# Optimization experiments

Hardware: AMD Instinct MI355X
Metric: run time of the kernel (lower is better)

## Reference

```python
import jax, jax.numpy as jnp
import numpy as np

INPUT_SIZE = 512
HIDDEN = 1024
N_QP = 64
M_QP = 128
QP_ITER = 50
MIN_EIG = 0.01
N_P = N_QP * (N_QP + 1) // 2              # 2080
N_H = M_QP * N_QP                          # 8192
N_OUT = N_P + N_QP + N_H + M_QP            # 10464
BATCH = 1024


def setup_inputs() -> dict:
    key = jax.random.key(0)
    ks = jax.random.split(key, 4)
    s = lambda fan_in: np.float32(1.0 / np.sqrt(fan_in))
    return {
        "x": jax.random.normal(ks[0], (BATCH, INPUT_SIZE), jnp.float32),
        "W1": jax.random.normal(ks[1], (INPUT_SIZE, HIDDEN), jnp.float32) * s(INPUT_SIZE),
        "b1": jnp.zeros((HIDDEN,), jnp.float32),
        "W2": jax.random.normal(ks[2], (HIDDEN, HIDDEN), jnp.float32) * s(HIDDEN),
        "b2": jnp.zeros((HIDDEN,), jnp.float32),
        "W3": jax.random.normal(ks[3], (HIDDEN, N_OUT), jnp.float32) * s(HIDDEN),
        "b3": jnp.zeros((N_OUT,), jnp.float32),
    }


def _make_psd(p):
    # p: (bs, n(n+1)/2) packed row-major lower triangle of Cholesky factor L.
    # Diagonal entries (index i(i+1)/2 - 1) -> sqrt(min_eig) + softplus, so P = L L' is PSD.
    bs = p.shape[0]
    i = jnp.arange(1, N_QP + 1)
    diag_idx = i * (i + 1) // 2 - 1
    p = p.at[:, diag_idx].set(np.float32(np.sqrt(MIN_EIG)) + jax.nn.softplus(p[:, diag_idx]))
    r, c = jnp.tril_indices(N_QP)
    L = jnp.zeros((bs, N_QP, N_QP), p.dtype).at[:, r, c].set(p)
    return jnp.einsum('bik,bjk->bij', L, L)


def _forward(x, W1, b1, W2, b2, W3, b3):
    # MLP generating QP parameters (P, q, H, b)
    h = jax.nn.relu(x @ W1 + b1)
    h = jax.nn.relu(h @ W2 + b2)
    out = h @ W3 + b3                               # (bs, N_OUT)
    P_params = out[:, :N_P]
    q = out[:, N_P:N_P + N_QP]                      # (bs, n)
    H = out[:, N_P + N_QP:N_P + N_QP + N_H].reshape(-1, M_QP, N_QP)  # (bs, m, n)
    b = out[:, N_P + N_QP + N_H:]                   # (bs, m)
    P = _make_psd(P_params)                         # (bs, n, n)

    # Step sizes: tau = sigma = 0.9 / ||H||_2, spectral norm via 10 fixed power iterations
    v = jnp.ones((x.shape[0], N_QP), x.dtype) / np.float32(np.sqrt(N_QP))
    for _ in range(10):
        w = jnp.einsum('bmn,bm->bn', H, jnp.einsum('bmn,bn->bm', H, v))
        v = w / (jnp.linalg.norm(w, axis=1, keepdims=True) + 1e-12)
    sn = jnp.linalg.norm(jnp.einsum('bmn,bn->bm', H, v), axis=1) + 1e-6
    tau = (0.9 / sn)[:, None]                       # (bs, 1) primal step
    sig = tau                                       # dual step

    # Precompute (I + tau P)^{-1} once; fixed across PDHG iterations
    eye = jnp.eye(N_QP, dtype=x.dtype)
    Minv = jnp.linalg.inv(eye[None] + tau[:, :, None] * P)

    x0 = jnp.zeros((x.shape[0], N_QP), x.dtype)
    lam0 = jnp.zeros((x.shape[0], M_QP), x.dtype)

    def step(carry, _):
        xp, xbar, lam = carry
        lam = jax.nn.relu(lam - sig * (jnp.einsum('bmn,bn->bm', H, xbar) + b))
        xn = jnp.einsum('bnk,bk->bn', Minv, xp + tau * (jnp.einsum('bmn,bm->bn', H, lam) - q))
        return (xn, 2.0 * xn - xp, lam), None

    (xs, _, _), _ = jax.lax.scan(step, (x0, x0, lam0), None, length=QP_ITER)
    return xs  # (bs, n_qp): last primal iterate, matching solver(...)[1][:, -1, :]


def reference(x, W1, b1, W2, b2, W3, b3):
    return _forward(x, W1, b1, W2, b2, W3, b3)
```

## Files before the change

### kernel.cpp

```cpp
#include <hip/hip_runtime.h>
#include <cstdint>

typedef unsigned short u16;
typedef __attribute__((ext_vector_type(8))) short short8;
typedef __attribute__((ext_vector_type(4))) float floatx4;
typedef __attribute__((ext_vector_type(4))) float f4;

#define NQP   64
#define MQP   128
#define NP    2080
#define NHH   8192
#define NOUT  10464
#define NOUTP 10496

__device__ __forceinline__ float b2f(u16 u) {
  union { unsigned int i; float f; } v; v.i = ((unsigned int)u) << 16; return v.f;
}
__device__ __forceinline__ u16 f2b(float f) {
  union { float f; unsigned int i; } v; v.f = f;
  unsigned int r = v.i + 0x7fffu + ((v.i >> 16) & 1u);
  return (u16)(r >> 16);
}

__global__ __launch_bounds__(256) void detect_dtype(const u16* __restrict__ w,
                                                    int* __restrict__ flag) {
  __shared__ int cnt;
  if (threadIdx.x == 0) cnt = 0;
  __syncthreads();
  int c = 0;
  for (int i = threadIdx.x; i < 16384; i += 256) {
    const int e = (w[i] >> 7) & 0xFF;
    if (e >= 130 || e <= 90) ++c;
  }
  atomicAdd(&cnt, c);
  __syncthreads();
  if (threadIdx.x == 0) flag[0] = (cnt > 3000) ? 1 : 0;
}

__device__ __forceinline__ u16 load_elem_bf16(const void* p, size_t idx, int isf32) {
  return isf32 ? f2b(((const float*)p)[idx]) : ((const u16*)p)[idx];
}

__global__ __launch_bounds__(256) void convert_bf16(const void* __restrict__ in,
                                                    u16* __restrict__ out, int n,
                                                    const int* __restrict__ flag) {
  const int isf = flag[0];
  for (int i = blockIdx.x * 256 + threadIdx.x; i < n; i += gridDim.x * 256)
    out[i] = load_elem_bf16(in, i, isf);
}

__global__ __launch_bounds__(256) void conv_biases(const void* __restrict__ b1,
                                                   const void* __restrict__ b2,
                                                   const void* __restrict__ b3,
                                                   float* __restrict__ bf1,
                                                   float* __restrict__ bf2,
                                                   float* __restrict__ bf3,
                                                   const int* __restrict__ flag) {
  const int isf = flag[0];
  const int i = blockIdx.x * 256 + threadIdx.x;
  if (i < 1024) {
    bf1[i] = isf ? ((const float*)b1)[i] : b2f(((const u16*)b1)[i]);
  } else if (i < 2048) {
    const int j = i - 1024;
    bf2[j] = isf ? ((const float*)b2)[j] : b2f(((const u16*)b2)[j]);
  } else if (i < 2048 + NOUT) {
    const int j = i - 2048;
    bf3[j] = isf ? ((const float*)b3)[j] : b2f(((const u16*)b3)[j]);
  }
}

__global__ __launch_bounds__(256) void transpose_all(const void* __restrict__ W1,
                                                     const void* __restrict__ W2,
                                                     const void* __restrict__ W3,
                                                     u16* __restrict__ W1t,
                                                     u16* __restrict__ W2t,
                                                     u16* __restrict__ W3t,
                                                     const int* __restrict__ flag) {
  const int bx = blockIdx.x, by = blockIdx.y;
  const void* in; u16* out; int K, N, Npad, bxo;
  if (bx < 32)      { in = W1; out = W1t; K = 512;  N = 1024; Npad = 1024;  bxo = 0;
                      if (by >= 16) return; }
  else if (bx < 64) { in = W2; out = W2t; K = 1024; N = 1024; Npad = 1024;  bxo = 32; }
  else              { in = W3; out = W3t; K = 1024; N = NOUT; Npad = NOUTP; bxo = 64; }
  __shared__ u16 tile[32][33];
  const int isf = flag[0];
  const int n0 = (bx - bxo) * 32, k0 = by * 32;
  const int tx = threadIdx.x & 31, ty = threadIdx.x >> 5;
// ... 100 lines not shown
__global__ __launch_bounds__(256) void gemm_bt64(const u16* __restrict__ Ahi, const u16* __restrict__ Alo,
                                                 const u16* __restrict__ Bt,  const float* __restrict__ bias,
                                                 u16* __restrict__ Chi, u16* __restrict__ Clo,
                                                 int N, int K) {
  __shared__ __align__(16) u16 lA[64 * 32];
  __shared__ __align__(16) u16 lAlo[64 * 32];
  __shared__ __align__(16) u16 lB[64 * 32];
  const int tile_n = blockIdx.x * 64;
  const int tile_m = blockIdx.y * 64;
  const int lane = threadIdx.x & 63;
  const int wv   = threadIdx.x >> 6;
  const int wm = (wv & 1) * 32;
  const int wn = (wv >> 1) * 32;
  const int sr = lane >> 2;
  const int sk = (lane & 3) * 8;
  floatx4 acc[2][2] = {};

  for (int k0 = 0; k0 < K; k0 += 32) {
    {
      const int r = wv * 16 + sr;
      gload_lds16(Ahi + (size_t)(tile_m + r) * K + k0 + sk, lA + wv * 512);
      if (HAS_LO)
        gload_lds16(Alo + (size_t)(tile_m + r) * K + k0 + sk, lAlo + wv * 512);
      gload_lds16(Bt + (size_t)(tile_n + r) * K + k0 + sk, lB + wv * 512);
    }
    __syncthreads();
    const int ro = lane & 15;
    const int qo = (lane >> 4) * 8;
    short8 af[2], bfr[2], al[2];
#pragma unroll
    for (int i = 0; i < 2; ++i) af[i] = *(const short8*)(lA + (wm + i * 16 + ro) * 32 + qo);
#pragma unroll
    for (int j = 0; j < 2; ++j) bfr[j] = *(const short8*)(lB + (wn + j * 16 + ro) * 32 + qo);
    if (HAS_LO) {
#pragma unroll
      for (int i = 0; i < 2; ++i) al[i] = *(const short8*)(lAlo + (wm + i * 16 + ro) * 32 + qo);
    }
#pragma unroll
    for (int i = 0; i < 2; ++i)
#pragma unroll
      for (int j = 0; j < 2; ++j) {
        acc[i][j] = __builtin_amdgcn_mfma_f32_16x16x32_bf16(af[i], bfr[j], acc[i][j], 0, 0, 0);
        if (HAS_LO)
          acc[i][j] = __builtin_amdgcn_mfma_f32_16x16x32_bf16(al[i], bfr[j], acc[i][j], 0, 0, 0);
      }
    __syncthreads();
  }

  const int colb = tile_n + wn + (lane & 15);
  const int rowb = tile_m + wm + (lane >> 4) * 4;
#pragma unroll
  for (int j = 0; j < 2; ++j) {
    const int col = colb + j * 16;
    const float bv = bias[col];
#pragma unroll
    for (int i = 0; i < 2; ++i) {
#pragma unroll
      for (int v = 0; v < 4; ++v) {
        const int row = rowb + i * 16 + v;
        float val = acc[i][j][v] + bv;
        val = fmaxf(val, 0.f);
        const u16 hi = f2b(val);
        Chi[(size_t)row * N + col] = hi;
        if (EPI == 0) {
          const float lo = val - b2f(hi);
          Clo[(size_t)row * N + col] = f2b(lo);
        }
      }
    }
  }
}

__device__ __forceinline__ f4 ld4s(const float* p) { return *(const f4*)p; }
__device__ __forceinline__ void st4s(float* p, f4 v) { *(f4*)p = v; }
__device__ __forceinline__ float dot4(f4 a, f4 b) {
  return fmaf(a.x, b.x, fmaf(a.y, b.y, fmaf(a.z, b.z, a.w * b.w)));
}
__device__ __forceinline__ f4 shx4(f4 v, int m) {
  f4 r;
  r.x = __shfl_xor(v.x, m, 64); r.y = __shfl_xor(v.y, m, 64);
  r.z = __shfl_xor(v.z, m, 64); r.w = __shfl_xor(v.w, m, 64);
  return r;
}
__device__ __forceinline__ int hQ(int m, int g) {
  return (m << 6) + (((g ^ (m & 15))) << 2);
}

__global__ __launch_bounds__(256, 4) void qp_solve(const float* __restrict__ outbuf,
                                                   void* __restrict__ xs,
                                                   const int* __restrict__ flag) {
  __shared__ __align__(16) float H_s[8192];
  __shared__ __align__(16) float lam_s[128];
  __shared__ __align__(16) float b_s[128];
  __shared__ __align__(16) float part_s[4][64];
  __shared__ __align__(16) float rhs_s[64];
  __shared__ __align__(16) float xb_s[64];
  __shared__ __align__(16) float xp_s[64];
  __shared__ __align__(16) float q_s[64];
  __shared__ __align__(16) float buf2[2][64];
  __shared__ float tau_sh;

  const int t = threadIdx.x;
  const int w = t >> 6, l = t & 63;
  const int am = 32 * w + (l >> 1), as = l & 1;
  const int bg = l & 15, bc = l >> 4;
  const int ci = 16 * w + (l >> 2), cc = l & 3;
  const int isf = flag[0];
  const float* ob = outbuf + (size_t)blockIdx.x * NOUT;

  float* Ld = H_s;
  float* ps = H_s + 4352;
  for (int e = t; e < 4352; e += 256) Ld[e] = 0.f;
  for (int e = t; e < NP; e += 256) ps[e] = ob[e];
  if (t < 64) q_s[t] = ob[NP + t];
  if (t >= 128 && t < 256) b_s[t - 128] = ob[NP + NQP + NHH + (t - 128)];
  __syncthreads();
  if (t < 64) {
    const int i = t + 1;
    const int d = i * (i + 1) / 2 - 1;
    const float xv = ps[d];
    ps[d] = 0.1f + (fmaxf(xv, 0.f) + log1pf(expf(-fabsf(xv))));
  }
  __syncthreads();
  for (int e = t; e < NP; e += 256) {
    int i = (int)((sqrtf(8.f * (float)e + 1.f) - 1.f) * 0.5f);
    while ((i + 1) * (i + 2) / 2 <= e) ++i;
    while (i * (i + 1) / 2 > e) --i;
    const int j = e - i * (i + 1) / 2;
    Ld[i * 68 + j] = ps[e];
  }
  __syncthreads();

  float M[16];
#pragma unroll
  for (int jj = 0; jj < 16; ++jj) M[jj] = 0.f;
#pragma unroll
  for (int h = 0; h < 2; ++h) {
    f4 Lr[8];
#pragma unroll
    for (int g = 0; g < 8; ++g) Lr[g] = ld4s(&Ld[ci * 68 + (h * 8 + g) * 4]);
#pragma unroll
    for (int jj = 0; jj < 16; ++jj) {
      const int j = 16 * cc + jj;
      float s = 0.f;
#pragma unroll
      for (int g = 0; g < 8; ++g) s += dot4(Lr[g], ld4s(&Ld[j * 68 + (h * 8 + g) * 4]));
      M[jj] += s;
    }
  }
  __syncthreads();

  for (int e = t; e < NHH; e += 256) {
    const int m = e >> 6, n = e & 63;
    H_s[hQ(m, n >> 2) + (n & 3)] = ob[NP + NQP + e];
  }
  if (t < 64) xb_s[t] = 0.125f;
  __syncthreads();

  for (int pi = 0; pi < 10; ++pi) {
    {
      float s = 0.f;
#pragma unroll
      for (int k = 0; k < 8; ++k) {
        const int g = 8 * as + k;
        s += dot4(ld4s(&H_s[hQ(am, g)]), ld4s(&xb_s[4 * g]));
      }
      s += __shfl_xor(s, 1, 64);
      if (as == 0) lam_s[am] = s;
    }
    __syncthreads();
    {
      f4 u = {0.f, 0.f, 0.f, 0.f};
#pragma unroll
      for (int k = 0; k < 8; ++k) {
        const int m = 32 * w + 8 * bc + k;
        u += ld4s(&H_s[hQ(m, bg)]) * lam_s[m];
      }
      u += shx4(u, 16); u += shx4(u, 32);
      if (l < 16) st4s(&part_s[w][4 * bg], u);
    }
    __syncthreads();
    if (t < 64) {
      const float u = part_s[0][t] + part_s[1][t] + part_s[2][t] + part_s[3][t];
      float ss = u * u;
#pragma unroll
      for (int o = 1; o <= 32; o <<= 1) ss += __shfl_xor(ss, o, 64);
      xb_s[t] = u / (sqrtf(ss) + 1e-12f);
    }
    __syncthreads();
  }
  {
    float s = 0.f;
#pragma unroll
    for (int k = 0; k < 8; ++k) {
      const int g = 8 * as + k;
      s += dot4(ld4s(&H_s[hQ(am, g)]), ld4s(&xb_s[4 * g]));
    }
    s += __shfl_xor(s, 1, 64);
    if (as == 0) lam_s[am] = s;
  }
  __syncthreads();
  if (t < 64) {
    const float a = lam_s[t], bb = lam_s[t + 64];
    float ss = a * a + bb * bb;
#pragma unroll
    for (int o = 1; o <= 32; o <<= 1) ss += __shfl_xor(ss, o, 64);
    if (t == 0) tau_sh = 0.9f / (sqrtf(ss) + 1e-6f);
  }
  __syncthreads();
  const float tau = tau_sh;

#pragma unroll
  for (int jj = 0; jj < 16; ++jj)
    M[jj] = tau * M[jj] + ((16 * cc + jj == ci) ? 1.0f : 0.0f);

  if (ci == 0) {
#pragma unroll
    for (int jj = 0; jj < 16; ++jj) buf2[0][16 * cc + jj] = M[jj];
  }
  __syncthreads();
#pragma unroll
  for (int k = 0; k < 64; ++k) {
    const int kb = k & 1;
    const int kc = k >> 4;
    const float d = 1.0f / buf2[kb][k];
    f4 rv[4];
#pragma unroll
    for (int u = 0; u < 4; ++u) rv[u] = ld4s(&buf2[kb][16 * cc + 4 * u]);
    const float f = __shfl(M[k & 15], (l & 60) | kc, 64);
    if (ci == k) {
#pragma unroll
      for (int jj = 0; jj < 16; ++jj) M[jj] = rv[jj >> 2][jj & 3] * d;
      if (cc == kc) M[k & 15] = d;
    } else {
#pragma unroll
      for (int jj = 0; jj < 16; ++jj)
        M[jj] = fmaf(-f, rv[jj >> 2][jj & 3] * d, M[jj]);
      if (cc == kc) M[k & 15] = -f * d;
    }
    if (k < 63 && ci == k + 1) {
#pragma unroll
      for (int jj = 0; jj < 16; ++jj) buf2[1 - kb][16 * cc + jj] = M[jj];
    }
    __syncthreads();
  }

  float c0;
  {
    float acc = 0.f;
#pragma unroll
    for (int u = 0; u < 4; ++u) {
      const f4 qv = ld4s(&q_s[16 * cc + 4 * u]);
      acc = fmaf(M[4 * u + 0], qv.x, acc);
      acc = fmaf(M[4 * u + 1], qv.y, acc);
      acc = fmaf(M[4 * u + 2], qv.z, acc);
      acc = fmaf(M[4 * u + 3], qv.w, acc);
    }
    acc += __shfl_xor(acc, 1, 64);
    acc += __shfl_xor(acc, 2, 64);
    c0 = tau * acc;
  }

  if (t < 64) { xb_s[t] = 0.f; xp_s[t] = 0.f; }
  float lam = 0.f, xpr = 0.f;
  const float br = b_s[am];
  __syncthreads();

  for (int it = 0; it < 50; ++it) {
    {
      float s = 0.f;
#pragma unroll
      for (int k = 0; k < 8; ++k) {
        const int g = 8 * as + k;
        s += dot4(ld4s(&H_s[hQ(am, g)]), ld4s(&xb_s[4 * g]));
      }
      s += __shfl_xor(s, 1, 64);
      lam = fmaxf(lam - tau * (s + br), 0.f);
      if (as == 0) lam_s[am] = lam;
    }
    __syncthreads();
    {
      f4 u = {0.f, 0.f, 0.f, 0.f};
#pragma unroll
      for (int k = 0; k < 8; ++k) {
        const int m = 32 * w + 8 * bc + k;
        u += ld4s(&H_s[hQ(m, bg)]) * lam_s[m];
      }
      u += shx4(u, 16); u += shx4(u, 32);
      if (l < 16) st4s(&part_s[w][4 * bg], u);
    }
    __syncthreads();
    if (t < 64) {
      const float uu = part_s[0][t] + part_s[1][t] + part_s[2][t] + part_s[3][t];
      rhs_s[t] = xp_s[t] + tau * uu;
    }
    __syncthreads();
    {
      float acc = 0.f;
#pragma unroll
      for (int u = 0; u < 4; ++u) {
        const f4 rv = ld4s(&rhs_s[16 * cc + 4 * u]);
        acc = fmaf(M[4 * u + 0], rv.x, acc);
        acc = fmaf(M[4 * u + 1], rv.y, acc);
        acc = fmaf(M[4 * u + 2], rv.z, acc);
        acc = fmaf(M[4 * u + 3], rv.w, acc);
      }
      acc += __shfl_xor(acc, 1, 64);
      acc += __shfl_xor(acc, 2, 64);
      if (cc == 0) {
        const float xn = acc - c0;
        xp_s[ci] = xn;
        xb_s[ci] = 2.f * xn - xpr;
        xpr = xn;
      }
    }
    __syncthreads();
  }

  if (cc == 0) {
    const size_t oi = (size_t)blockIdx.x * NQP + ci;
    if (isf) ((float*)xs)[oi] = xpr;
    else     ((u16*)xs)[oi]   = f2b(xpr);
  }
}

extern "C" void kernel_launch(void* const* d_in, const int* in_sizes, int n_in,
                              void* d_out, int out_size, void* d_ws, size_t ws_size,
                              hipStream_t stream) {
  const void* x  = d_in[0];
  const void* W1 = d_in[1];
  const void* b1 = d_in[2];
  const void* W2 = d_in[3];
  const void* b2 = d_in[4];
  const void* W3 = d_in[5];
  const void* b3 = d_in[6];

  char* ws = (char*)d_ws;
  size_t off = 0;
  auto take = [&](size_t bytes) -> char* {
    char* r = ws + off;
    off += (bytes + 255) & ~(size_t)255;
    return r;
  };
  int*   flag = (int*)take(256);
  float* bf1  = (float*)take(1024 * 4);
  float* bf2  = (float*)take(1024 * 4);
  float* bf3  = (float*)take((size_t)NOUT * 4);
  u16*   W3t  = (u16*)take((size_t)NOUTP * 1024 * 2);
  u16*   h2hi = (u16*)take(1024ull * 1024 * 2);
  char*  region = take(1024ull * NOUT * 4);
  float* outf = (float*)region;
  u16* xb   = (u16*)(region + 0);
  u16* W1t  = (u16*)(region + (1u << 20));
  u16* W2t  = (u16*)(region + (2u << 20));
  u16* h1hi = (u16*)(region + (4u << 20));
  u16* h1lo = (u16*)(region + (6u << 20));
  (void)ws_size; (void)in_sizes; (void)n_in; (void)out_size;

  detect_dtype<<<dim3(1), 256, 0, stream>>>((const u16*)W1, flag);

  convert_bf16<<<dim3(512), 256, 0, stream>>>(x, xb, 1024 * 512, flag);
  conv_biases<<<dim3(49), 256, 0, stream>>>(b1, b2, b3, bf1, bf2, bf3, flag);
  transpose_all<<<dim3(392, 32), 256, 0, stream>>>(W1, W2, W3, W1t, W2t, W3t, flag);

  gemm_bt64<0, false><<<dim3(16, 16), 256, 0, stream>>>(xb, nullptr, W1t, bf1,
                                                        h1hi, h1lo, 1024, 512);
  gemm_bt64<2, true><<<dim3(16, 16), 256, 0, stream>>>(h1hi, h1lo, W2t, bf2,
                                                       h2hi, nullptr, 1024, 1024);
  gemm_bt<1, false><<<dim3(NOUTP / 128, 8), 256, 0, stream>>>(h2hi, nullptr, W3t, bf3,
                                                              nullptr, nullptr, outf, 1024, NOUT, 1024);
  qp_solve<<<dim3(1024), 256, 0, stream>>>(outf, d_out, flag);
}
```

Measured before the change: 466.6 us.

## Store QP constraint matrix H in LDS as bf16 to double occupancy

The per-batch constraint matrix H is converted to bf16 and stored in shared memory with a new XOR swizzle. This halves its LDS footprint so launch bounds can be raised from 4 to 8 blocks per CU. The smaller scratch buffers (b_s, rhs_s) are removed by reusing lam_s and reading b straight from global memory. The cost is extra conversion work in the inner loops and reduced precision in H across the 50 PDHG iterations and the power iteration, which may drift from the fp32 reference.

```diff
diff --git a/kernel.cpp b/kernel.cpp
--- a/kernel.cpp
+++ b/kernel.cpp
@@ -3,6 +3,7 @@
 
 typedef unsigned short u16;
 typedef __attribute__((ext_vector_type(8))) short short8;
+typedef __attribute__((ext_vector_type(4))) short shortx4;
 typedef __attribute__((ext_vector_type(4))) float floatx4;
 typedef __attribute__((ext_vector_type(4))) float f4;
 
@@ -269,18 +270,24 @@
   r.z = __shfl_xor(v.z, m, 64); r.w = __shfl_xor(v.w, m, 64);
   return r;
 }
-__device__ __forceinline__ int hQ(int m, int g) {
-  return (m << 6) + (((g ^ (m & 15))) << 2);
-}
-
-__global__ __launch_bounds__(256, 4) void qp_solve(const float* __restrict__ outbuf,
+__device__ __forceinline__ float dot8h(short8 h, f4 a, f4 b) {
+  float s = b2f((u16)h[0]) * a.x;
+  s = fmaf(b2f((u16)h[1]), a.y, s);
+  s = fmaf(b2f((u16)h[2]), a.z, s);
+  s = fmaf(b2f((u16)h[3]), a.w, s);
+  s = fmaf(b2f((u16)h[4]), b.x, s);
+  s = fmaf(b2f((u16)h[5]), b.y, s);
+  s = fmaf(b2f((u16)h[6]), b.z, s);
+  s = fmaf(b2f((u16)h[7]), b.w, s);
+  return s;
+}
+
+__global__ __launch_bounds__(256, 8) void qp_solve(const float* __restrict__ outbuf,
                                                    void* __restrict__ xs,
                                                    const int* __restrict__ flag) {
-  __shared__ __align__(16) float H_s[8192];
+  __shared__ __align__(16) float Hreg[4352];
   __shared__ __align__(16) float lam_s[128];
-  __shared__ __align__(16) float b_s[128];
   __shared__ __align__(16) float part_s[4][64];
-  __shared__ __align__(16) float rhs_s[64];
   __shared__ __align__(16) float xb_s[64];
   __shared__ __align__(16) float xp_s[64];
   __shared__ __align__(16) float q_s[64];
@@ -294,27 +301,23 @@
   const int ci = 16 * w + (l >> 2), cc = l & 3;
   const int isf = flag[0];
   const float* ob = outbuf + (size_t)blockIdx.x * NOUT;
-
-  float* Ld = H_s;
-  float* ps = H_s + 4352;
+  u16* Hb = (u16*)Hreg;
+
+  float* Ld = Hreg;
   for (int e = t; e < 4352; e += 256) Ld[e] = 0.f;
-  for (int e = t; e < NP; e += 256) ps[e] = ob[e];
   if (t < 64) q_s[t] = ob[NP + t];
-  if (t >= 128 && t < 256) b_s[t - 128] = ob[NP + NQP + NHH + (t - 128)];
-  __syncthreads();
-  if (t < 64) {
-    const int i = t + 1;
-    const int d = i * (i + 1) / 2 - 1;
-    const float xv = ps[d];
-    ps[d] = 0.1f + (fmaxf(xv, 0.f) + log1pf(expf(-fabsf(xv))));
-  }
   __syncthreads();
   for (int e = t; e < NP; e += 256) {
     int i = (int)((sqrtf(8.f * (float)e + 1.f) - 1.f) * 0.5f);
     while ((i + 1) * (i + 2) / 2 <= e) ++i;
     while (i * (i + 1) / 2 > e) --i;
     const int j = e - i * (i + 1) / 2;
-    Ld[i * 68 + j] = ps[e];
+    Ld[i * 68 + j] = ob[e];
+  }
+  __syncthreads();
+  if (t < 64) {
+    const float xv = Ld[t * 68 + t];
+    Ld[t * 68 + t] = 0.1f + (fmaxf(xv, 0.f) + log1pf(expf(-fabsf(xv))));
   }
   __syncthreads();
 
@@ -337,20 +340,28 @@
   }
   __syncthreads();
 
-  for (int e = t; e < NHH; e += 256) {
-    const int m = e >> 6, n = e & 63;
-    H_s[hQ(m, n >> 2) + (n & 3)] = ob[NP + NQP + e];
+  for (int e = t; e < 4096; e += 256) {
+    const int m = e >> 5;
+    const int n = (e & 31) * 2;
+    const float f0 = ob[NP + NQP + m * 64 + n];
+    const float f1 = ob[NP + NQP + m * 64 + n + 1];
+    const int pc = (n >> 3) ^ (m & 7);
+    const int idx = (m << 6) + (pc << 3) + (n & 7);
+    *(unsigned int*)(Hb + idx) = (unsigned int)f2b(f0) | ((unsigned int)f2b(f1) << 16);
   }
   if (t < 64) xb_s[t] = 0.125f;
   __syncthreads();
+
+  const int am64 = am << 6, ax7 = am & 7;
 
   for (int pi = 0; pi < 10; ++pi) {
     {
       float s = 0.f;
 #pragma unroll
-      for (int k = 0; k < 8; ++k) {
-        const int g = 8 * as + k;
-        s += dot4(ld4s(&H_s[hQ(am, g)]), ld4s(&xb_s[4 * g]));
+      for (int c4 = 0; c4 < 4; ++c4) {
+        const int c = 4 * as + c4;
+        const short8 hv = *(const short8*)(Hb + am64 + ((c ^ ax7) << 3));
+        s += dot8h(hv, ld4s(&xb_s[8 * c]), ld4s(&xb_s[8 * c + 4]));
       }
       s += __shfl_xor(s, 1, 64);
       if (as == 0) lam_s[am] = s;
@@ -361,7 +372,12 @@
 #pragma unroll
       for (int k = 0; k < 8; ++k) {
         const int m = 32 * w + 8 * bc + k;
-        u += ld4s(&H_s[hQ(m, bg)]) * lam_s[m];
+        const shortx4 hv = *(const shortx4*)(Hb + (m << 6) + (((bg >> 1) ^ k) << 3) + ((bg & 1) << 2));
+        const float lm = lam_s[m];
+        u.x = fmaf(b2f((u16)hv.x), lm, u.x);
+        u.y = fmaf(b2f((u16)hv.y), lm, u.y);
+        u.z = fmaf(b2f((u16)hv.z), lm, u.z);
+        u.w = fmaf(b2f((u16)hv.w), lm, u.w);
       }
       u += shx4(u, 16); u += shx4(u, 32);
       if (l < 16) st4s(&part_s[w][4 * bg], u);
@@ -379,9 +395,10 @@
   {
     float s = 0.f;
 #pragma unroll
-    for (int k = 0; k < 8; ++k) {
-      const int g = 8 * as + k;
-      s += dot4(ld4s(&H_s[hQ(am, g)]), ld4s(&xb_s[4 * g]));
+    for (int c4 = 0; c4 < 4; ++c4) {
+      const int c = 4 * as + c4;
+      const short8 hv = *(const short8*)(Hb + am64 + ((c ^ ax7) << 3));
+      s += dot8h(hv, ld4s(&xb_s[8 * c]), ld4s(&xb_s[8 * c + 4]));
     }
     s += __shfl_xor(s, 1, 64);
     if (as == 0) lam_s[am] = s;
@@ -450,16 +467,17 @@
 
   if (t < 64) { xb_s[t] = 0.f; xp_s[t] = 0.f; }
   float lam = 0.f, xpr = 0.f;
-  const float br = b_s[am];
+  const float br = ob[NP + NQP + NHH + am];
   __syncthreads();
 
   for (int it = 0; it < 50; ++it) {
     {
       float s = 0.f;
 #pragma unroll
-      for (int k = 0; k < 8; ++k) {
-        const int g = 8 * as + k;
-        s += dot4(ld4s(&H_s[hQ(am, g)]), ld4s(&xb_s[4 * g]));
+      for (int c4 = 0; c4 < 4; ++c4) {
+        const int c = 4 * as + c4;
+        const short8 hv = *(const short8*)(Hb + am64 + ((c ^ ax7) << 3));
+        s += dot8h(hv, ld4s(&xb_s[8 * c]), ld4s(&xb_s[8 * c + 4]));
       }
       s += __shfl_xor(s, 1, 64);
       lam = fmaxf(lam - tau * (s + br), 0.f);
@@ -471,7 +489,12 @@
 #pragma unroll
       for (int k = 0; k < 8; ++k) {
         const int m = 32 * w + 8 * bc + k;
-        u += ld4s(&H_s[hQ(m, bg)]) * lam_s[m];
+        const shortx4 hv = *(const shortx4*)(Hb + (m << 6) + (((bg >> 1) ^ k) << 3) + ((bg & 1) << 2));
+        const float lm = lam_s[m];
+        u.x = fmaf(b2f((u16)hv.x), lm, u.x);
+        u.y = fmaf(b2f((u16)hv.y), lm, u.y);
+        u.z = fmaf(b2f((u16)hv.z), lm, u.z);
+        u.w = fmaf(b2f((u16)hv.w), lm, u.w);
       }
       u += shx4(u, 16); u += shx4(u, 32);
       if (l < 16) st4s(&part_s[w][4 * bg], u);
@@ -479,14 +502,14 @@
     __syncthreads();
     if (t < 64) {
       const float uu = part_s[0][t] + part_s[1][t] + part_s[2][t] + part_s[3][t];
-      rhs_s[t] = xp_s[t] + tau * uu;
+      lam_s[t] = xp_s[t] + tau * uu;
     }
     __syncthreads();
     {
       float acc = 0.f;
 #pragma unroll
       for (int u = 0; u < 4; ++u) {
-        const f4 rv = ld4s(&rhs_s[16 * cc + 4 * u]);
+        const f4 rv = ld4s(&lam_s[16 * cc + 4 * u]);
         acc = fmaf(M[4 * u + 0], rv.x, acc);
         acc = fmaf(M[4 * u + 1], rv.y, acc);
         acc = fmaf(M[4 * u + 2], rv.z, acc);
```

Result: slower. 582.3 us (+24.8%).

## Solve two QP problems per block to amortize barriers and raise ILP

Applied to the files above, without the earlier changes.

The QP solver kernel now processes two batch samples per 256-thread block, interleaving their matrix-vector products, Gauss-Jordan inversion and PDHG iterations. The goal is to halve the number of barrier-bound serial steps per sample and give each thread two independent dependency chains. In exchange, shared memory per block doubles to about 66KB and register pressure rises, which cuts occupancy (launch bounds drop to 2 blocks per SM). The grid also shrinks to 512 blocks, which can leave CUs underused.

```diff
diff --git a/kernel.cpp b/kernel.cpp
--- a/kernel.cpp
+++ b/kernel.cpp
@@ -273,19 +273,20 @@
   return (m << 6) + (((g ^ (m & 15))) << 2);
 }
 
-__global__ __launch_bounds__(256, 4) void qp_solve(const float* __restrict__ outbuf,
-                                                   void* __restrict__ xs,
-                                                   const int* __restrict__ flag) {
-  __shared__ __align__(16) float H_s[8192];
-  __shared__ __align__(16) float lam_s[128];
-  __shared__ __align__(16) float b_s[128];
-  __shared__ __align__(16) float part_s[4][64];
-  __shared__ __align__(16) float rhs_s[64];
-  __shared__ __align__(16) float xb_s[64];
-  __shared__ __align__(16) float xp_s[64];
-  __shared__ __align__(16) float q_s[64];
-  __shared__ __align__(16) float buf2[2][64];
-  __shared__ float tau_sh;
+__global__ __launch_bounds__(256, 2) void qp_solve2(const float* __restrict__ outbuf,
+                                                    void* __restrict__ xs,
+                                                    const int* __restrict__ flag) {
+  __shared__ __align__(16) float H0_s[8192];
+  __shared__ __align__(16) float H1_s[8192];
+  __shared__ __align__(16) float lam0_s[128], lam1_s[128];
+  __shared__ __align__(16) float b0_s[128], b1_s[128];
+  __shared__ __align__(16) float part0_s[4][64], part1_s[4][64];
+  __shared__ __align__(16) float rhs0_s[64], rhs1_s[64];
+  __shared__ __align__(16) float xb0_s[64], xb1_s[64];
+  __shared__ __align__(16) float xp0_s[64], xp1_s[64];
+  __shared__ __align__(16) float q0_s[64], q1_s[64];
+  __shared__ __align__(16) float buf20[2][64], buf21[2][64];
+  __shared__ float tau0_sh, tau1_sh;
 
   const int t = threadIdx.x;
   const int w = t >> 6, l = t & 63;
@@ -293,20 +294,28 @@
   const int bg = l & 15, bc = l >> 4;
   const int ci = 16 * w + (l >> 2), cc = l & 3;
   const int isf = flag[0];
-  const float* ob = outbuf + (size_t)blockIdx.x * NOUT;
-
-  float* Ld = H_s;
-  float* ps = H_s + 4352;
-  for (int e = t; e < 4352; e += 256) Ld[e] = 0.f;
-  for (int e = t; e < NP; e += 256) ps[e] = ob[e];
-  if (t < 64) q_s[t] = ob[NP + t];
-  if (t >= 128 && t < 256) b_s[t - 128] = ob[NP + NQP + NHH + (t - 128)];
+  const float* ob0 = outbuf + (size_t)(2 * blockIdx.x) * NOUT;
+  const float* ob1 = outbuf + (size_t)(2 * blockIdx.x + 1) * NOUT;
+
+  float* Ld0 = H0_s;                 float* ps0 = H0_s + 4352;
+  float* Ld1 = H1_s;                 float* ps1 = H1_s + 4352;
+  for (int e = t; e < 4352; e += 256) { Ld0[e] = 0.f; Ld1[e] = 0.f; }
+  for (int e = t; e < NP; e += 256) { ps0[e] = ob0[e]; ps1[e] = ob1[e]; }
+  if (t < 64)        q0_s[t] = ob0[NP + t];
+  else if (t < 128)  q1_s[t - 64] = ob1[NP + (t - 64)];
+  if (t < 128) b0_s[t] = ob0[NP + NQP + NHH + t];
+  else         b1_s[t - 128] = ob1[NP + NQP + NHH + (t - 128)];
   __syncthreads();
   if (t < 64) {
     const int i = t + 1;
     const int d = i * (i + 1) / 2 - 1;
-    const float xv = ps[d];
-    ps[d] = 0.1f + (fmaxf(xv, 0.f) + log1pf(expf(-fabsf(xv))));
+    const float xv = ps0[d];
+    ps0[d] = 0.1f + (fmaxf(xv, 0.f) + log1pf(expf(-fabsf(xv))));
+  } else if (t < 128) {
+    const int i = (t - 64) + 1;
+    const int d = i * (i + 1) / 2 - 1;
+    const float xv = ps1[d];
+    ps1[d] = 0.1f + (fmaxf(xv, 0.f) + log1pf(expf(-fabsf(xv))));
   }
   __syncthreads();
   for (int e = t; e < NP; e += 256) {
@@ -314,200 +323,289 @@
     while ((i + 1) * (i + 2) / 2 <= e) ++i;
     while (i * (i + 1) / 2 > e) --i;
     const int j = e - i * (i + 1) / 2;
-    Ld[i * 68 + j] = ps[e];
-  }
-  __syncthreads();
-
-  float M[16];
-#pragma unroll
-  for (int jj = 0; jj < 16; ++jj) M[jj] = 0.f;
+    Ld0[i * 68 + j] = ps0[e];
+    Ld1[i * 68 + j] = ps1[e];
+  }
+  __syncthreads();
+
+  float M0[16], M1[16];
+#pragma unroll
+  for (int jj = 0; jj < 16; ++jj) { M0[jj] = 0.f; M1[jj] = 0.f; }
 #pragma unroll
   for (int h = 0; h < 2; ++h) {
     f4 Lr[8];
 #pragma unroll
-    for (int g = 0; g < 8; ++g) Lr[g] = ld4s(&Ld[ci * 68 + (h * 8 + g) * 4]);
+    for (int g = 0; g < 8; ++g) Lr[g] = ld4s(&Ld0[ci * 68 + (h * 8 + g) * 4]);
 #pragma unroll
     for (int jj = 0; jj < 16; ++jj) {
       const int j = 16 * cc + jj;
       float s = 0.f;
 #pragma unroll
-      for (int g = 0; g < 8; ++g) s += dot4(Lr[g], ld4s(&Ld[j * 68 + (h * 8 + g) * 4]));
-      M[jj] += s;
+      for (int g = 0; g < 8; ++g) s += dot4(Lr[g], ld4s(&Ld0[j * 68 + (h * 8 + g) * 4]));
+      M0[jj] += s;
+    }
+  }
+#pragma unroll
+  for (int h = 0; h < 2; ++h) {
+    f4 Lr[8];
+#pragma unroll
+    for (int g = 0; g < 8; ++g) Lr[g] = ld4s(&Ld1[ci * 68 + (h * 8 + g) * 4]);
+#pragma unroll
+    for (int jj = 0; jj < 16; ++jj) {
+      const int j = 16 * cc + jj;
+      float s = 0.f;
+#pragma unroll
+      for (int g = 0; g < 8; ++g) s += dot4(Lr[g], ld4s(&Ld1[j * 68 + (h * 8 + g) * 4]));
+      M1[jj] += s;
     }
   }
   __syncthreads();
 
   for (int e = t; e < NHH; e += 256) {
     const int m = e >> 6, n = e & 63;
-    H_s[hQ(m, n >> 2) + (n & 3)] = ob[NP + NQP + e];
-  }
-  if (t < 64) xb_s[t] = 0.125f;
+    const int qi = hQ(m, n >> 2) + (n & 3);
+    H0_s[qi] = ob0[NP + NQP + e];
+    H1_s[qi] = ob1[NP + NQP + e];
+  }
+  if (t < 64)       xb0_s[t] = 0.125f;
+  else if (t < 128) xb1_s[t - 64] = 0.125f;
   __syncthreads();
 
   for (int pi = 0; pi < 10; ++pi) {
     {
-      float s = 0.f;
+      float s0 = 0.f, s1 = 0.f;
 #pragma unroll
       for (int k = 0; k < 8; ++k) {
         const int g = 8 * as + k;
-        s += dot4(ld4s(&H_s[hQ(am, g)]), ld4s(&xb_s[4 * g]));
-      }
-      s += __shfl_xor(s, 1, 64);
-      if (as == 0) lam_s[am] = s;
+        s0 += dot4(ld4s(&H0_s[hQ(am, g)]), ld4s(&xb0_s[4 * g]));
+        s1 += dot4(ld4s(&H1_s[hQ(am, g)]), ld4s(&xb1_s[4 * g]));
+      }
+      s0 += __shfl_xor(s0, 1, 64);
+      s1 += __shfl_xor(s1, 1, 64);
+      if (as == 0) { lam0_s[am] = s0; lam1_s[am] = s1; }
     }
     __syncthreads();
     {
-      f4 u = {0.f, 0.f, 0.f, 0.f};
+      f4 u0 = {0.f, 0.f, 0.f, 0.f}, u1 = {0.f, 0.f, 0.f, 0.f};
 #pragma unroll
       for (int k = 0; k < 8; ++k) {
         const int m = 32 * w + 8 * bc + k;
-        u += ld4s(&H_s[hQ(m, bg)]) * lam_s[m];
-      }
-      u += shx4(u, 16); u += shx4(u, 32);
-      if (l < 16) st4s(&part_s[w][4 * bg], u);
+        u0 += ld4s(&H0_s[hQ(m, bg)]) * lam0_s[m];
+        u1 += ld4s(&H1_s[hQ(m, bg)]) * lam1_s[m];
+      }
+      u0 += shx4(u0, 16); u0 += shx4(u0, 32);
+      u1 += shx4(u1, 16); u1 += shx4(u1, 32);
+      if (l < 16) { st4s(&part0_s[w][4 * bg], u0); st4s(&part1_s[w][4 * bg], u1); }
     }
     __syncthreads();
     if (t < 64) {
-      const float u = part_s[0][t] + part_s[1][t] + part_s[2][t] + part_s[3][t];
+      const float u = part0_s[0][t] + part0_s[1][t] + part0_s[2][t] + part0_s[3][t];
       float ss = u * u;
 #pragma unroll
       for (int o = 1; o <= 32; o <<= 1) ss += __shfl_xor(ss, o, 64);
-      xb_s[t] = u / (sqrtf(ss) + 1e-12f);
+      xb0_s[t] = u / (sqrtf(ss) + 1e-12f);
+    } else if (t < 128) {
+      const int tt = t - 64;
+      const float u = part1_s[0][tt] + part1_s[1][tt] + part1_s[2][tt] + part1_s[3][tt];
+      float ss = u * u;
+#pragma unroll
+      for (int o = 1; o <= 32; o <<= 1) ss += __shfl_xor(ss, o, 64);
+      xb1_s[tt] = u / (sqrtf(ss) + 1e-12f);
     }
     __syncthreads();
   }
   {
-    float s = 0.f;
+    float s0 = 0.f, s1 = 0.f;
 #pragma unroll
     for (int k = 0; k < 8; ++k) {
       const int g = 8 * as + k;
-      s += dot4(ld4s(&H_s[hQ(am, g)]), ld4s(&xb_s[4 * g]));
-    }
-    s += __shfl_xor(s, 1, 64);
-    if (as == 0) lam_s[am] = s;
+      s0 += dot4(ld4s(&H0_s[hQ(am, g)]), ld4s(&xb0_s[4 * g]));
+      s1 += dot4(ld4s(&H1_s[hQ(am, g)]), ld4s(&xb1_s[4 * g]));
+    }
+    s0 += __shfl_xor(s0, 1, 64);
+    s1 += __shfl_xor(s1, 1, 64);
+    if (as == 0) { lam0_s[am] = s0; lam1_s[am] = s1; }
   }
   __syncthreads();
   if (t < 64) {
-    const float a = lam_s[t], bb = lam_s[t + 64];
+    const float a = lam0_s[t], bb = lam0_s[t + 64];
     float ss = a * a + bb * bb;
 #pragma unroll
     for (int o = 1; o <= 32; o <<= 1) ss += __shfl_xor(ss, o, 64);
-    if (t == 0) tau_sh = 0.9f / (sqrtf(ss) + 1e-6f);
-  }
-  __syncthreads();
-  const float tau = tau_sh;
-
-#pragma unroll
-  for (int jj = 0; jj < 16; ++jj)
-    M[jj] = tau * M[jj] + ((16 * cc + jj == ci) ? 1.0f : 0.0f);
+    if (t == 0) tau0_sh = 0.9f / (sqrtf(ss) + 1e-6f);
+  } else if (t < 128) {
+    const int tt = t - 64;
+    const float a = lam1_s[tt], bb = lam1_s[tt + 64];
+    float ss = a * a + bb * bb;
+#pragma unroll
+    for (int o = 1; o <= 32; o <<= 1) ss += __shfl_xor(ss, o, 64);
+    if (tt == 0) tau1_sh = 0.9f / (sqrtf(ss) + 1e-6f);
+  }
+  __syncthreads();
+  const float tau0 = tau0_sh, tau1 = tau1_sh;
+
+#pragma unroll
+  for (int jj = 0; jj < 16; ++jj) {
+    const float ind = (16 * cc + jj == ci) ? 1.0f : 0.0f;
+    M0[jj] = tau0 * M0[jj] + ind;
+    M1[jj] = tau1 * M1[jj] + ind;
+  }
 
   if (ci == 0) {
 #pragma unroll
-    for (int jj = 0; jj < 16; ++jj) buf2[0][16 * cc + jj] = M[jj];
+    for (int jj = 0; jj < 16; ++jj) {
+      buf20[0][16 * cc + jj] = M0[jj];
+      buf21[0][16 * cc + jj] = M1[jj];
+    }
   }
   __syncthreads();
 #pragma unroll
   for (int k = 0; k < 64; ++k) {
     const int kb = k & 1;
     const int kc = k >> 4;
-    const float d = 1.0f / buf2[kb][k];
-    f4 rv[4];
-#pragma unroll
-    for (int u = 0; u < 4; ++u) rv[u] = ld4s(&buf2[kb][16 * cc + 4 * u]);
-    const float f = __shfl(M[k & 15], (l & 60) | kc, 64);
+    const float d0 = 1.0f / buf20[kb][k];
+    const float d1 = 1.0f / buf21[kb][k];
+    f4 rv0[4], rv1[4];
+#pragma unroll
+    for (int u = 0; u < 4; ++u) {
+      rv0[u] = ld4s(&buf20[kb][16 * cc + 4 * u]);
+      rv1[u] = ld4s(&buf21[kb][16 * cc + 4 * u]);
+    }
+    const float f0 = __shfl(M0[k & 15], (l & 60) | kc, 64);
+    const float f1 = __shfl(M1[k & 15], (l & 60) | kc, 64);
     if (ci == k) {
 #pragma unroll
-      for (int jj = 0; jj < 16; ++jj) M[jj] = rv[jj >> 2][jj & 3] * d;
-      if (cc == kc) M[k & 15] = d;
+      for (int jj = 0; jj < 16; ++jj) {
+        M0[jj] = rv0[jj >> 2][jj & 3] * d0;
+        M1[jj] = rv1[jj >> 2][jj & 3] * d1;
+      }
+      if (cc == kc) { M0[k & 15] = d0; M1[k & 15] = d1; }
     } else {
 #pragma unroll
-      for (int jj = 0; jj < 16; ++jj)
-        M[jj] = fmaf(-f, rv[jj >> 2][jj & 3] * d, M[jj]);
-      if (cc == kc) M[k & 15] = -f * d;
+      for (int jj = 0; jj < 16; ++jj) {
+        M0[jj] = fmaf(-f0, rv0[jj >> 2][jj & 3] * d0, M0[jj]);
+        M1[jj] = fmaf(-f1, rv1[jj >> 2][jj & 3] * d1, M1[jj]);
+      }
+      if (cc == kc) { M0[k & 15] = -f0 * d0; M1[k & 15] = -f1 * d1; }
     }
     if (k < 63 && ci == k + 1) {
 #pragma unroll
-      for (int jj = 0; jj < 16; ++jj) buf2[1 - kb][16 * cc + jj] = M[jj];
-    }
-    __syncthreads();
-  }
-
-  float c0;
+      for (int jj = 0; jj < 16; ++jj) {
+        buf20[1 - kb][16 * cc + jj] = M0[jj];
+        buf21[1 - kb][16 * cc + jj] = M1[jj];
+      }
+    }
+    __syncthreads();
+  }
+
+  float c00, c01;
   {
-    float acc = 0.f;
+    float a0 = 0.f, a1 = 0.f;
 #pragma unroll
     for (int u = 0; u < 4; ++u) {
-      const f4 qv = ld4s(&q_s[16 * cc + 4 * u]);
-      acc = fmaf(M[4 * u + 0], qv.x, acc);
-      acc = fmaf(M[4 * u + 1], qv.y, acc);
-      acc = fmaf(M[4 * u + 2], qv.z, acc);
-      acc = fmaf(M[4 * u + 3], qv.w, acc);
-    }
-    acc += __shfl_xor(acc, 1, 64);
-    acc += __shfl_xor(acc, 2, 64);
-    c0 = tau * acc;
-  }
-
-  if (t < 64) { xb_s[t] = 0.f; xp_s[t] = 0.f; }
-  float lam = 0.f, xpr = 0.f;
-  const float br = b_s[am];
+      const f4 qv0 = ld4s(&q0_s[16 * cc + 4 * u]);
+      const f4 qv1 = ld4s(&q1_s[16 * cc + 4 * u]);
+      a0 = fmaf(M0[4 * u + 0], qv0.x, a0);
+      a0 = fmaf(M0[4 * u + 1], qv0.y, a0);
+      a0 = fmaf(M0[4 * u + 2], qv0.z, a0);
+      a0 = fmaf(M0[4 * u + 3], qv0.w, a0);
+      a1 = fmaf(M1[4 * u + 0], qv1.x, a1);
+      a1 = fmaf(M1[4 * u + 1], qv1.y, a1);
+      a1 = fmaf(M1[4 * u + 2], qv1.z, a1);
+      a1 = fmaf(M1[4 * u + 3], qv1.w, a1);
+    }
+    a0 += __shfl_xor(a0, 1, 64); a0 += __shfl_xor(a0, 2, 64);
+    a1 += __shfl_xor(a1, 1, 64); a1 += __shfl_xor(a1, 2, 64);
+    c00 = tau0 * a0;
+    c01 = tau1 * a1;
+  }
+
+  if (t < 64)       { xb0_s[t] = 0.f; xp0_s[t] = 0.f; }
+  else if (t < 128) { xb1_s[t - 64] = 0.f; xp1_s[t - 64] = 0.f; }
+  float lam0 = 0.f, lam1 = 0.f, xpr0 = 0.f, xpr1 = 0.f;
+  const float br0 = b0_s[am];
+  const float br1 = b1_s[am];
   __syncthreads();
 
   for (int it = 0; it < 50; ++it) {
     {
-      float s = 0.f;
+      float s0 = 0.f, s1 = 0.f;
 #pragma unroll
       for (int k = 0; k < 8; ++k) {
         const int g = 8 * as + k;
-        s += dot4(ld4s(&H_s[hQ(am, g)]), ld4s(&xb_s[4 * g]));
-      }
-      s += __shfl_xor(s, 1, 64);
-      lam = fmaxf(lam - tau * (s + br), 0.f);
-      if (as == 0) lam_s[am] = lam;
+        s0 += dot4(ld4s(&H0_s[hQ(am, g)]), ld4s(&xb0_s[4 * g]));
+        s1 += dot4(ld4s(&H1_s[hQ(am, g)]), ld4s(&xb1_s[4 * g]));
+      }
+      s0 += __shfl_xor(s0, 1, 64);
+      s1 += __shfl_xor(s1, 1, 64);
+      lam0 = fmaxf(lam0 - tau0 * (s0 + br0), 0.f);
+      lam1 = fmaxf(lam1 - tau1 * (s1 + br1), 0.f);
+      if (as == 0) { lam0_s[am] = lam0; lam1_s[am] = lam1; }
     }
     __syncthreads();
     {
-      f4 u = {0.f, 0.f, 0.f, 0.f};
+      f4 u0 = {0.f, 0.f, 0.f, 0.f}, u1 = {0.f, 0.f, 0.f, 0.f};
 #pragma unroll
       for (int k = 0; k < 8; ++k) {
         const int m = 32 * w + 8 * bc + k;
-        u += ld4s(&H_s[hQ(m, bg)]) * lam_s[m];
-      }
-      u += shx4(u, 16); u += shx4(u, 32);
-      if (l < 16) st4s(&part_s[w][4 * bg], u);
+        u0 += ld4s(&H0_s[hQ(m, bg)]) * lam0_s[m];
+        u1 += ld4s(&H1_s[hQ(m, bg)]) * lam1_s[m];
+      }
+      u0 += shx4(u0, 16); u0 += shx4(u0, 32);
+      u1 += shx4(u1, 16); u1 += shx4(u1, 32);
+      if (l < 16) { st4s(&part0_s[w][4 * bg], u0); st4s(&part1_s[w][4 * bg], u1); }
     }
     __syncthreads();
     if (t < 64) {
-      const float uu = part_s[0][t] + part_s[1][t] + part_s[2][t] + part_s[3][t];
-      rhs_s[t] = xp_s[t] + tau * uu;
+      const float uu = part0_s[0][t] + part0_s[1][t] + part0_s[2][t] + part0_s[3][t];
+      rhs0_s[t] = xp0_s[t] + tau0 * uu;
+    } else if (t < 128) {
+      const int tt = t - 64;
+      const float uu = part1_s[0][tt] + part1_s[1][tt] + part1_s[2][tt] + part1_s[3][tt];
+      rhs1_s[tt] = xp1_s[tt] + tau1 * uu;
     }
     __syncthreads();
     {
-      float acc = 0.f;
+      float a0 = 0.f, a1 = 0.f;
 #pragma unroll
       for (int u = 0; u < 4; ++u) {
-        const f4 rv = ld4s(&rhs_s[16 * cc + 4 * u]);
-        acc = fmaf(M[4 * u + 0], rv.x, acc);
-        acc = fmaf(M[4 * u + 1], rv.y, acc);
-        acc = fmaf(M[4 * u + 2], rv.z, acc);
-        acc = fmaf(M[4 * u + 3], rv.w, acc);
-      }
-      acc += __shfl_xor(acc, 1, 64);
-      acc += __shfl_xor(acc, 2, 64);
+        const f4 rv0 = ld4s(&rhs0_s[16 * cc + 4 * u]);
+        const f4 rv1 = ld4s(&rhs1_s[16 * cc + 4 * u]);
+        a0 = fmaf(M0[4 * u + 0], rv0.x, a0);
+        a0 = fmaf(M0[4 * u + 1], rv0.y, a0);
+        a0 = fmaf(M0[4 * u + 2], rv0.z, a0);
+        a0 = fmaf(M0[4 * u + 3], rv0.w, a0);
+        a1 = fmaf(M1[4 * u + 0], rv1.x, a1);
+        a1 = fmaf(M1[4 * u + 1], rv1.y, a1);
+        a1 = fmaf(M1[4 * u + 2], rv1.z, a1);
+        a1 = fmaf(M1[4 * u + 3], rv1.w, a1);
+      }
+      a0 += __shfl_xor(a0, 1, 64); a0 += __shfl_xor(a0, 2, 64);
+      a1 += __shfl_xor(a1, 1, 64); a1 += __shfl_xor(a1, 2, 64);
       if (cc == 0) {
-        const float xn = acc - c0;
-        xp_s[ci] = xn;
-        xb_s[ci] = 2.f * xn - xpr;
-        xpr = xn;
+        const float xn0 = a0 - c00;
+        xp0_s[ci] = xn0;
+        xb0_s[ci] = 2.f * xn0 - xpr0;
+        xpr0 = xn0;
+        const float xn1 = a1 - c01;
+        xp1_s[ci] = xn1;
+        xb1_s[ci] = 2.f * xn1 - xpr1;
+        xpr1 = xn1;
       }
     }
     __syncthreads();
   }
 
   if (cc == 0) {
-    const size_t oi = (size_t)blockIdx.x * NQP + ci;
-    if (isf) ((float*)xs)[oi] = xpr;
-    else     ((u16*)xs)[oi]   = f2b(xpr);
+    const size_t oi0 = (size_t)(2 * blockIdx.x) * NQP + ci;
+    const size_t oi1 = oi0 + NQP;
+    if (isf) {
+      ((float*)xs)[oi0] = xpr0;
+      ((float*)xs)[oi1] = xpr1;
+    } else {
+      ((u16*)xs)[oi0] = f2b(xpr0);
+      ((u16*)xs)[oi1] = f2b(xpr1);
+    }
   }
 }
 
@@ -556,5 +654,5 @@
                                                        h2hi, nullptr, 1024, 1024);
   gemm_bt<1, false><<<dim3(NOUTP / 128, 8), 256, 0, stream>>>(h2hi, nullptr, W3t, bf3,
                                                               nullptr, nullptr, outf, 1024, NOUT, 1024);
-  qp_solve<<<dim3(1024), 256, 0, stream>>>(outf, d_out, flag);
-}
+  qp_solve2<<<dim3(512), 256, 0, stream>>>(outf, d_out, flag);
+}
```

Result: slower. 526.3 us (+12.8%).

## Widen QP solve block to 512 threads and split H matvecs across eight waves

Applied to the files above, without the earlier changes.

Doubles the qp_solve block from 256 to 512 threads. The H·x and Hᵀ·λ products in the power iteration and the PDHG loop are now split over 8 waves, with 4 lanes per row and 8 partial sums. The Cholesky product, the 64x64 inverse and the M·rhs step stay on the first 256 threads, so the upper half idles during those phases and only joins the barriers. The aim is to shorten the latency-bound per-iteration matvecs, at the cost of more barrier participants and the launch-bounds change to (512, 8) limiting registers per thread.

```diff
diff --git a/kernel.cpp b/kernel.cpp
--- a/kernel.cpp
+++ b/kernel.cpp
@@ -273,13 +273,13 @@
   return (m << 6) + (((g ^ (m & 15))) << 2);
 }
 
-__global__ __launch_bounds__(256, 4) void qp_solve(const float* __restrict__ outbuf,
+__global__ __launch_bounds__(512, 8) void qp_solve(const float* __restrict__ outbuf,
                                                    void* __restrict__ xs,
                                                    const int* __restrict__ flag) {
   __shared__ __align__(16) float H_s[8192];
   __shared__ __align__(16) float lam_s[128];
   __shared__ __align__(16) float b_s[128];
-  __shared__ __align__(16) float part_s[4][64];
+  __shared__ __align__(16) float part_s[8][64];
   __shared__ __align__(16) float rhs_s[64];
   __shared__ __align__(16) float xb_s[64];
   __shared__ __align__(16) float xp_s[64];
@@ -288,17 +288,18 @@
   __shared__ float tau_sh;
 
   const int t = threadIdx.x;
-  const int w = t >> 6, l = t & 63;
-  const int am = 32 * w + (l >> 1), as = l & 1;
+  const int wv = t >> 6, l = t & 63;
+  const int ar = t >> 2, aq = t & 3;
   const int bg = l & 15, bc = l >> 4;
-  const int ci = 16 * w + (l >> 2), cc = l & 3;
+  const int w4 = t >> 6;
+  const int ci = 16 * w4 + (l >> 2), cc = l & 3;
   const int isf = flag[0];
   const float* ob = outbuf + (size_t)blockIdx.x * NOUT;
 
   float* Ld = H_s;
   float* ps = H_s + 4352;
-  for (int e = t; e < 4352; e += 256) Ld[e] = 0.f;
-  for (int e = t; e < NP; e += 256) ps[e] = ob[e];
+  for (int e = t; e < 4352; e += 512) Ld[e] = 0.f;
+  for (int e = t; e < NP; e += 512) ps[e] = ob[e];
   if (t < 64) q_s[t] = ob[NP + t];
   if (t >= 128 && t < 256) b_s[t - 128] = ob[NP + NQP + NHH + (t - 128)];
   __syncthreads();
@@ -309,7 +310,7 @@
     ps[d] = 0.1f + (fmaxf(xv, 0.f) + log1pf(expf(-fabsf(xv))));
   }
   __syncthreads();
-  for (int e = t; e < NP; e += 256) {
+  for (int e = t; e < NP; e += 512) {
     int i = (int)((sqrtf(8.f * (float)e + 1.f) - 1.f) * 0.5f);
     while ((i + 1) * (i + 2) / 2 <= e) ++i;
     while (i * (i + 1) / 2 > e) --i;
@@ -321,23 +322,25 @@
   float M[16];
 #pragma unroll
   for (int jj = 0; jj < 16; ++jj) M[jj] = 0.f;
-#pragma unroll
-  for (int h = 0; h < 2; ++h) {
-    f4 Lr[8];
-#pragma unroll
-    for (int g = 0; g < 8; ++g) Lr[g] = ld4s(&Ld[ci * 68 + (h * 8 + g) * 4]);
-#pragma unroll
-    for (int jj = 0; jj < 16; ++jj) {
-      const int j = 16 * cc + jj;
-      float s = 0.f;
-#pragma unroll
-      for (int g = 0; g < 8; ++g) s += dot4(Lr[g], ld4s(&Ld[j * 68 + (h * 8 + g) * 4]));
-      M[jj] += s;
-    }
-  }
-  __syncthreads();
-
-  for (int e = t; e < NHH; e += 256) {
+  if (t < 256) {
+#pragma unroll
+    for (int h = 0; h < 2; ++h) {
+      f4 Lr[8];
+#pragma unroll
+      for (int g = 0; g < 8; ++g) Lr[g] = ld4s(&Ld[ci * 68 + (h * 8 + g) * 4]);
+#pragma unroll
+      for (int jj = 0; jj < 16; ++jj) {
+        const int j = 16 * cc + jj;
+        float s = 0.f;
+#pragma unroll
+        for (int g = 0; g < 8; ++g) s += dot4(Lr[g], ld4s(&Ld[j * 68 + (h * 8 + g) * 4]));
+        M[jj] += s;
+      }
+    }
+  }
+  __syncthreads();
+
+  for (int e = t; e < NHH; e += 512) {
     const int m = e >> 6, n = e & 63;
     H_s[hQ(m, n >> 2) + (n & 3)] = ob[NP + NQP + e];
   }
@@ -348,27 +351,29 @@
     {
       float s = 0.f;
 #pragma unroll
-      for (int k = 0; k < 8; ++k) {
-        const int g = 8 * as + k;
-        s += dot4(ld4s(&H_s[hQ(am, g)]), ld4s(&xb_s[4 * g]));
+      for (int k = 0; k < 4; ++k) {
+        const int g = 4 * aq + k;
+        s += dot4(ld4s(&H_s[hQ(ar, g)]), ld4s(&xb_s[4 * g]));
       }
       s += __shfl_xor(s, 1, 64);
-      if (as == 0) lam_s[am] = s;
+      s += __shfl_xor(s, 2, 64);
+      if (aq == 0) lam_s[ar] = s;
     }
     __syncthreads();
     {
       f4 u = {0.f, 0.f, 0.f, 0.f};
 #pragma unroll
-      for (int k = 0; k < 8; ++k) {
-        const int m = 32 * w + 8 * bc + k;
+      for (int k = 0; k < 4; ++k) {
+        const int m = 16 * wv + 4 * bc + k;
         u += ld4s(&H_s[hQ(m, bg)]) * lam_s[m];
       }
       u += shx4(u, 16); u += shx4(u, 32);
-      if (l < 16) st4s(&part_s[w][4 * bg], u);
+      if (l < 16) st4s(&part_s[wv][4 * bg], u);
     }
     __syncthreads();
     if (t < 64) {
-      const float u = part_s[0][t] + part_s[1][t] + part_s[2][t] + part_s[3][t];
+      const float u = ((part_s[0][t] + part_s[1][t]) + (part_s[2][t] + part_s[3][t])) +
+                      ((part_s[4][t] + part_s[5][t]) + (part_s[6][t] + part_s[7][t]));
       float ss = u * u;
 #pragma unroll
       for (int o = 1; o <= 32; o <<= 1) ss += __shfl_xor(ss, o, 64);
@@ -379,21 +384,21 @@
   {
     float s = 0.f;
 #pragma unroll
-    for (int k = 0; k < 8; ++k) {
-      const int g = 8 * as + k;
-      s += dot4(ld4s(&H_s[hQ(am, g)]), ld4s(&xb_s[4 * g]));
+    for (int k = 0; k < 4; ++k) {
+      const int g = 4 * aq + k;
+      s += dot4(ld4s(&H_s[hQ(ar, g)]), ld4s(&xb_s[4 * g]));
     }
     s += __shfl_xor(s, 1, 64);
-    if (as == 0) lam_s[am] = s;
-  }
-  __syncthreads();
-  if (t < 64) {
-    const float a = lam_s[t], bb = lam_s[t + 64];
-    float ss = a * a + bb * bb;
+    s += __shfl_xor(s, 2, 64);
+    float ss = (aq == 0) ? s * s : 0.f;
 #pragma unroll
     for (int o = 1; o <= 32; o <<= 1) ss += __shfl_xor(ss, o, 64);
-    if (t == 0) tau_sh = 0.9f / (sqrtf(ss) + 1e-6f);
-  }
+    if (l == 0) part_s[wv][0] = ss;
+  }
+  __syncthreads();
+  if (t == 0)
+    tau_sh = 0.9f / (sqrtf(((part_s[0][0] + part_s[1][0]) + (part_s[2][0] + part_s[3][0])) +
+                           ((part_s[4][0] + part_s[5][0]) + (part_s[6][0] + part_s[7][0]))) + 1e-6f);
   __syncthreads();
   const float tau = tau_sh;
 
@@ -401,39 +406,41 @@
   for (int jj = 0; jj < 16; ++jj)
     M[jj] = tau * M[jj] + ((16 * cc + jj == ci) ? 1.0f : 0.0f);
 
-  if (ci == 0) {
+  if (t < 256 && ci == 0) {
 #pragma unroll
     for (int jj = 0; jj < 16; ++jj) buf2[0][16 * cc + jj] = M[jj];
   }
   __syncthreads();
 #pragma unroll
   for (int k = 0; k < 64; ++k) {
-    const int kb = k & 1;
-    const int kc = k >> 4;
-    const float d = 1.0f / buf2[kb][k];
-    f4 rv[4];
-#pragma unroll
-    for (int u = 0; u < 4; ++u) rv[u] = ld4s(&buf2[kb][16 * cc + 4 * u]);
-    const float f = __shfl(M[k & 15], (l & 60) | kc, 64);
-    if (ci == k) {
-#pragma unroll
-      for (int jj = 0; jj < 16; ++jj) M[jj] = rv[jj >> 2][jj & 3] * d;
-      if (cc == kc) M[k & 15] = d;
-    } else {
-#pragma unroll
-      for (int jj = 0; jj < 16; ++jj)
-        M[jj] = fmaf(-f, rv[jj >> 2][jj & 3] * d, M[jj]);
-      if (cc == kc) M[k & 15] = -f * d;
-    }
-    if (k < 63 && ci == k + 1) {
-#pragma unroll
-      for (int jj = 0; jj < 16; ++jj) buf2[1 - kb][16 * cc + jj] = M[jj];
-    }
-    __syncthreads();
-  }
-
-  float c0;
-  {
+    if (t < 256) {
+      const int kb = k & 1;
+      const int kc = k >> 4;
+      const float d = 1.0f / buf2[kb][k];
+      f4 rv[4];
+#pragma unroll
+      for (int u = 0; u < 4; ++u) rv[u] = ld4s(&buf2[kb][16 * cc + 4 * u]);
+      const float f = __shfl(M[k & 15], (l & 60) | kc, 64);
+      if (ci == k) {
+#pragma unroll
+        for (int jj = 0; jj < 16; ++jj) M[jj] = rv[jj >> 2][jj & 3] * d;
+        if (cc == kc) M[k & 15] = d;
+      } else {
+#pragma unroll
+        for (int jj = 0; jj < 16; ++jj)
+          M[jj] = fmaf(-f, rv[jj >> 2][jj & 3] * d, M[jj]);
+        if (cc == kc) M[k & 15] = -f * d;
+      }
+      if (k < 63 && ci == k + 1) {
+#pragma unroll
+        for (int jj = 0; jj < 16; ++jj) buf2[1 - kb][16 * cc + jj] = M[jj];
+      }
+    }
+    __syncthreads();
+  }
+
+  float c0 = 0.f;
+  if (t < 256) {
     float acc = 0.f;
 #pragma unroll
     for (int u = 0; u < 4; ++u) {
@@ -450,39 +457,41 @@
 
   if (t < 64) { xb_s[t] = 0.f; xp_s[t] = 0.f; }
   float lam = 0.f, xpr = 0.f;
-  const float br = b_s[am];
+  const float br = b_s[ar & 127];
   __syncthreads();
 
   for (int it = 0; it < 50; ++it) {
     {
       float s = 0.f;
 #pragma unroll
-      for (int k = 0; k < 8; ++k) {
-        const int g = 8 * as + k;
-        s += dot4(ld4s(&H_s[hQ(am, g)]), ld4s(&xb_s[4 * g]));
+      for (int k = 0; k < 4; ++k) {
+        const int g = 4 * aq + k;
+        s += dot4(ld4s(&H_s[hQ(ar, g)]), ld4s(&xb_s[4 * g]));
       }
       s += __shfl_xor(s, 1, 64);
+      s += __shfl_xor(s, 2, 64);
       lam = fmaxf(lam - tau * (s + br), 0.f);
-      if (as == 0) lam_s[am] = lam;
+      if (aq == 0) lam_s[ar] = lam;
     }
     __syncthreads();
     {
       f4 u = {0.f, 0.f, 0.f, 0.f};
 #pragma unroll
-      for (int k = 0; k < 8; ++k) {
-        const int m = 32 * w + 8 * bc + k;
+      for (int k = 0; k < 4; ++k) {
+        const int m = 16 * wv + 4 * bc + k;
         u += ld4s(&H_s[hQ(m, bg)]) * lam_s[m];
       }
       u += shx4(u, 16); u += shx4(u, 32);
-      if (l < 16) st4s(&part_s[w][4 * bg], u);
+      if (l < 16) st4s(&part_s[wv][4 * bg], u);
     }
     __syncthreads();
     if (t < 64) {
-      const float uu = part_s[0][t] + part_s[1][t] + part_s[2][t] + part_s[3][t];
+      const float uu = ((part_s[0][t] + part_s[1][t]) + (part_s[2][t] + part_s[3][t])) +
+                       ((part_s[4][t] + part_s[5][t]) + (part_s[6][t] + part_s[7][t]));
       rhs_s[t] = xp_s[t] + tau * uu;
     }
     __syncthreads();
-    {
+    if (t < 256) {
       float acc = 0.f;
 #pragma unroll
       for (int u = 0; u < 4; ++u) {
@@ -504,7 +513,7 @@
     __syncthreads();
   }
 
-  if (cc == 0) {
+  if (t < 256 && cc == 0) {
     const size_t oi = (size_t)blockIdx.x * NQP + ci;
     if (isf) ((float*)xs)[oi] = xpr;
     else     ((u16*)xs)[oi]   = f2b(xpr);
@@ -556,5 +565,5 @@
                                                        h2hi, nullptr, 1024, 1024);
   gemm_bt<1, false><<<dim3(NOUTP / 128, 8), 256, 0, stream>>>(h2hi, nullptr, W3t, bf3,
                                                               nullptr, nullptr, outf, 1024, NOUT, 1024);
-  qp_solve<<<dim3(1024), 256, 0, stream>>>(outf, d_out, flag);
-}
+  qp_solve<<<dim3(1024), 512, 0, stream>>>(outf, d_out, flag);
+}
```

Result: slower. 550.4 us (+18.0%).
